# Kernel optimization log

Measured on AMD Instinct MI355X. Metric: run time of the kernel, lower is better.

Reference implementation:

```python
import jax, jax.numpy as jnp
import numpy as np

N, E, D, L = 50000, 600000, 128, 2  # nodes, edges, hidden_dim, num_gnn_layers
NEG_SLOPE = 0.2  # PyG GATv2Conv default negative_slope


def setup_inputs() -> dict:
    key = jax.random.key(0)
    ks = jax.random.split(key, 10)
    s = 1.0 / np.sqrt(D)
    return {
        "x": jax.random.normal(ks[0], (N, D), jnp.float32),
        "edge_index": jax.random.randint(ks[1], (2, E), 0, N, dtype=jnp.int32),
        # per-layer GATv2 params (stacked over L layers)
        "Wl": jax.random.normal(ks[2], (L, D, D), jnp.float32) * s,  # lin_l (source)
        "bl": jnp.zeros((L, D), jnp.float32),
        "Wr": jax.random.normal(ks[3], (L, D, D), jnp.float32) * s,  # lin_r (target)
        "br": jnp.zeros((L, D), jnp.float32),
        "att": jax.random.normal(ks[4], (L, D), jnp.float32) * s,
        "bias": jnp.zeros((L, D), jnp.float32),
        # shared residual Linear
        "W_res": jax.random.normal(ks[5], (D, D), jnp.float32) * s,
        "b_res": jnp.zeros((D,), jnp.float32),
    }


def reference(x, edge_index, Wl, bl, Wr, br, att, bias, W_res, b_res):
    n = x.shape[0]
    # add self loops (PyG GATv2Conv default add_self_loops=True)
    loops = jnp.arange(n, dtype=edge_index.dtype)
    src = jnp.concatenate([edge_index[0], loops])  # source j (messages)
    dst = jnp.concatenate([edge_index[1], loops])  # target i (aggregation)

    def conv(h, i):
        xl = h @ Wl[i] + bl[i]  # [N, D] source transform
        xr = h @ Wr[i] + br[i]  # [N, D] target transform
        m = xl[src] + xr[dst]   # [E+N, D] gathered edge messages
        e = jnp.einsum('ed,d->e', jnp.where(m > 0, m, NEG_SLOPE * m), att[i])
        # segment softmax over incoming edges of each destination node
        emax = jax.lax.stop_gradient(jax.ops.segment_max(e, dst, num_segments=n))
        ex = jnp.exp(e - emax[dst])
        denom = jax.ops.segment_sum(ex, dst, num_segments=n)
        alpha = ex / (denom[dst] + 1e-16)
        out = jax.ops.segment_sum(alpha[:, None] * xl[src], dst, num_segments=n)
        return out + bias[i]

    for i in range(Wl.shape[0]):
        x = jax.nn.relu(conv(x, i) + x @ W_res + b_res)
    return x
```

## Files before the change

kernel.cpp:

```cpp
#include <hip/hip_runtime.h>
#include <math.h>


#define DIM 128
#define NEG_SLOPE 0.2f
#define TPW 4

typedef __attribute__((ext_vector_type(8))) short short8;
typedef __attribute__((ext_vector_type(4))) float floatx4;
typedef __attribute__((ext_vector_type(2))) float f32x2;

static __device__ __forceinline__ unsigned short f2b(float f) {
    unsigned u = __float_as_uint(f);
    unsigned r = (u + 0x7FFFu + ((u >> 16) & 1u)) >> 16;
    return (unsigned short)r;
}
static __device__ __forceinline__ f32x2 cvt2(unsigned u) {
    f32x2 r;
    r.x = __uint_as_float(u << 16);
    r.y = __uint_as_float(u & 0xffff0000u);
    return r;
}
static __device__ __forceinline__ f32x2 pk_add(f32x2 a, f32x2 b) {
    f32x2 d;
    asm("v_pk_add_f32 %0, %1, %2" : "=v"(d) : "v"(a), "v"(b));
    return d;
}
static __device__ __forceinline__ f32x2 pk_mul(f32x2 a, f32x2 b) {
    f32x2 d;
    asm("v_pk_mul_f32 %0, %1, %2" : "=v"(d) : "v"(a), "v"(b));
    return d;
}
static __device__ __forceinline__ f32x2 pk_fma(f32x2 a, f32x2 b, f32x2 c) {
    f32x2 d;
    asm("v_pk_fma_f32 %0, %1, %2, %3" : "=v"(d) : "v"(a), "v"(b), "v"(c));
    return d;
}
static __device__ __forceinline__ f32x2 pk_abs2(f32x2 a) {
    f32x2 r;
    r.x = __builtin_fabsf(a.x);
    r.y = __builtin_fabsf(a.y);
    return r;
}

__global__ void k_init_counts(int* __restrict__ counts, int n) {
    int i = blockIdx.x * blockDim.x + threadIdx.x;
    if (i < n) counts[i] = 1;
}

__global__ void k_count(const int* __restrict__ dst, int E, int* __restrict__ counts) {
    int k = blockIdx.x * blockDim.x + threadIdx.x;
    if (k < E) atomicAdd(&counts[dst[k]], 1);
}

__global__ void k_scan1(const int* __restrict__ counts, int n,
                        int* __restrict__ rowptr, int* __restrict__ bsum) {
    __shared__ int s[256];
    int tid = threadIdx.x;
    int i = blockIdx.x * 256 + tid;
    int v = (i < n) ? counts[i] : 0;
    s[tid] = v;
    __syncthreads();
    for (int off = 1; off < 256; off <<= 1) {
        int t = (tid >= off) ? s[tid - off] : 0;
        __syncthreads();
        s[tid] += t;
        __syncthreads();
    }
    if (i < n) rowptr[i + 1] = s[tid];
    if (tid == 255) bsum[blockIdx.x] = s[255];
}

__global__ void k_scan2(int* __restrict__ bsum, int nb) {
    __shared__ int s[256];
    int tid = threadIdx.x;
    int v = (tid < nb) ? bsum[tid] : 0;
    s[tid] = v;
    __syncthreads();
    for (int off = 1; off < 256; off <<= 1) {
        int t = (tid >= off) ? s[tid - off] : 0;
        __syncthreads();
        s[tid] += t;
        __syncthreads();
    }
    if (tid < nb) bsum[tid] = s[tid];
}

__global__ void k_scan3(int* __restrict__ rowptr, const int* __restrict__ bsum,
                        int n, int* __restrict__ counts_to_cursors) {
    int i = blockIdx.x * 256 + threadIdx.x;
    if (i < n) {
        int add = (blockIdx.x > 0) ? bsum[blockIdx.x - 1] : 0;
        int cnt = counts_to_cursors[i];
        int v = rowptr[i + 1] + add;
        rowptr[i + 1] = v;
        counts_to_cursors[i] = v - cnt;
    }
    if (i == 0) rowptr[0] = 0;
}

__global__ void k_scatter(const int* __restrict__ src, const int* __restrict__ dst,
                          int E, int n, int* __restrict__ cur, int* __restrict__ srt) {
    int k = blockIdx.x * blockDim.x + threadIdx.x;
    int tot = E + n;
    if (k >= tot) return;
    int s, d;
    if (k < E) { s = src[k]; d = dst[k]; }
    else       { s = k - E;  d = s; }
    int p = atomicAdd(&cur[d], 1);
    srt[p] = s;
}

__global__ void k_pre(const float* __restrict__ Wl, const float* __restrict__ Wr,
                      const float* __restrict__ Wres, unsigned short* __restrict__ wfrag,
                      const float* __restrict__ h, unsigned short* __restrict__ hfrag,
                      int n, int ntiles) {
    int blk = blockIdx.x;
    if (blk < 48) {
        int idx = blk * 256 + threadIdx.x;
        int lane = idx & 63;
        int nr   = (idx >> 6) & 7;
        int ks   = (idx >> 9) & 3;
        int v    = idx >> 11;
        int sec = v % 3, l = v / 3;
        const float* W = (sec == 0) ? (Wl + l * DIM * DIM)
                       : (sec == 1) ? (Wr + l * DIM * DIM) : Wres;
        int nn = nr * 16 + (lane & 15);
        int k0 = ks * 32 + ((lane >> 4) << 3);
        ushort4 a, b;
        a.x = f2b(W[(k0 + 0) * DIM + nn]); a.y = f2b(W[(k0 + 1) * DIM + nn]);
        a.z = f2b(W[(k0 + 2) * DIM + nn]); a.w = f2b(W[(k0 + 3) * DIM + nn]);
        b.x = f2b(W[(k0 + 4) * DIM + nn]); b.y = f2b(W[(k0 + 5) * DIM + nn]);
        b.z = f2b(W[(k0 + 6) * DIM + nn]); b.w = f2b(W[(k0 + 7) * DIM + nn]);
        *(ushort4*)(wfrag + (size_t)idx * 8) = a;
        *(ushort4*)(wfrag + (size_t)idx * 8 + 4) = b;
    } else {
        int idx = (blk - 48) * 256 + threadIdx.x;
        if (idx >= ntiles * 256) return;
        int lane = idx & 63;
        int ks   = (idx >> 6) & 3;
        int tile = idx >> 8;
        int row  = tile * 16 + (lane & 15);
        int col0 = ks * 32 + ((lane >> 4) << 3);
        ushort4 a = {0, 0, 0, 0}, b = {0, 0, 0, 0};
        if (row < n) {
            float4 v0 = *(const float4*)(h + (size_t)row * DIM + col0);
            float4 v1 = *(const float4*)(h + (size_t)row * DIM + col0 + 4);
            a.x = f2b(v0.x); a.y = f2b(v0.y); a.z = f2b(v0.z); a.w = f2b(v0.w);
            b.x = f2b(v1.x); b.y = f2b(v1.y); b.z = f2b(v1.z); b.w = f2b(v1.w);
        }
        *(ushort4*)(hfrag + (size_t)idx * 8) = a;
        *(ushort4*)(hfrag + (size_t)idx * 8 + 4) = b;
    }
}

__global__ __launch_bounds__(256, 2) void k_gemm(
    const unsigned short* __restrict__ hfrag, const unsigned short* __restrict__ wfrag,
    const float* __restrict__ bl, const float* __restrict__ br, const float* __restrict__ bres,
    unsigned short* __restrict__ XLb, unsigned short* __restrict__ XRb,
    float* __restrict__ RES, int ntiles)
{
    int sec  = blockIdx.y;
    int lane = threadIdx.x & 63;
    int w    = threadIdx.x >> 6;

    const unsigned short* wbase = wfrag + (size_t)sec * (4 * 8 * 64 * 8);
    short8 bf[4][8];
#pragma unroll
    for (int ks = 0; ks < 4; ks++)
#pragma unroll
        for (int nr = 0; nr < 8; nr++)
            bf[ks][nr] = *(const short8*)(wbase + (((ks * 8 + nr) * 64 + lane) << 3));

    const float* bias = (sec == 0) ? bl : (sec == 1) ? br : bres;
    int colb = (lane >> 4) << 2;
    float4 bv[8];
#pragma unroll
    for (int nr = 0; nr < 8; nr++) bv[nr] = *(const float4*)(bias + nr * 16 + colb);

    int wid = blockIdx.x * 4 + w;
#pragma unroll
    for (int i = 0; i < TPW; i++) {
        int t = wid * TPW + i;
        if (t >= ntiles) break;
        short8 a[4];
#pragma unroll
        for (int ks = 0; ks < 4; ks++)
            a[ks] = *(const short8*)(hfrag + (((t * 4 + ks) * 64 + lane) << 3));
        floatx4 acc[8];
#pragma unroll
        for (int nr = 0; nr < 8; nr++) acc[nr] = (floatx4){0.f, 0.f, 0.f, 0.f};
#pragma unroll
        for (int ks = 0; ks < 4; ks++)
#pragma unroll
            for (int nr = 0; nr < 8; nr++)
                acc[nr] = __builtin_amdgcn_mfma_f32_16x16x32_bf16(bf[ks][nr], a[ks], acc[nr], 0, 0, 0);

        int row = t * 16 + (lane & 15);
        size_t rb = (size_t)row * DIM;
#pragma unroll
        for (int nr = 0; nr < 8; nr++) {
            float4 o;
            o.x = acc[nr][0] + bv[nr].x;
            o.y = acc[nr][1] + bv[nr].y;
            o.z = acc[nr][2] + bv[nr].z;
            o.w = acc[nr][3] + bv[nr].w;
            int col = nr * 16 + colb;
            if (sec == 2) {
                *(float4*)(RES + rb + col) = o;
            } else {
                ushort4 u;
                u.x = f2b(o.x); u.y = f2b(o.y); u.z = f2b(o.z); u.w = f2b(o.w);
                if (sec == 0) *(ushort4*)(XLb + rb + col) = u;
                else          *(ushort4*)(XRb + rb + col) = u;
            }
        }
    }
}

#define EDGE_LOGIT(K, JOFF)                                              \
    f32x2 v01_##K = cvt2(e##K.x), v23_##K = cvt2(e##K.y);                \
    f32x2 t01_##K = pk_add(v01_##K, x01);                                \
    f32x2 t23_##K = pk_add(v23_##K, x23);                                \
    f32x2 pp_##K = pk_mul(a6_01, t01_##K);                               \
    pp_##K = pk_fma(a4_01, pk_abs2(t01_##K), pp_##K);                    \
    pp_##K = pk_fma(a6_23, t23_##K, pp_##K);                             \
    pp_##K = pk_fma(a4_23, pk_abs2(t23_##K), pp_##K);                    \
    float p##K = pp_##K.x + pp_##K.y;                                    \
    p##K = (j + JOFF < se) ? p##K : -3.0e38f;

__global__ __launch_bounds__(256) void k_aggr(
    const unsigned short* __restrict__ XLb, const unsigned short* __restrict__ XRb,
    const float* __restrict__ RES, const float* __restrict__ att,
    const float* __restrict__ bias, const int* __restrict__ rowptr,
    const int* __restrict__ srt, float* __restrict__ outF,
    unsigned short* __restrict__ fragOut, int writeFrag, int n)
{
    int wave = threadIdx.x >> 6;
    int lane = threadIdx.x & 63;
    int node = blockIdx.x * 4 + wave;
    if (node >= n) return;
    int half = lane >> 5, sl = lane & 31;
    int d0 = sl << 2;

    float a0 = att[d0], a1 = att[d0 + 1], a2 = att[d0 + 2], a3 = att[d0 + 3];
    f32x2 a6_01 = {0.6f * a0, 0.6f * a1}, a6_23 = {0.6f * a2, 0.6f * a3};
    f32x2 a4_01 = {0.4f * a0, 0.4f * a1}, a4_23 = {0.4f * a2, 0.4f * a3};

    uint2 xru = *(const uint2*)(XRb + (size_t)node * DIM + d0);
    f32x2 x01 = cvt2(xru.x), x23 = cvt2(xru.y);

    int beg = rowptr[node], end = rowptr[node + 1];
    int len = end - beg;
    int hl = (len + 1) >> 1;
    int sb = beg + half * hl;
    int se = half ? end : (beg + hl);

    const uint2* R = (const uint2*)XLb;

    float m = -INFINITY, den = 0.f;
    float ax = 0.f, ay = 0.f, az = 0.f, aw = 0.f;

    for (int j = sb; j < se; j += 8) {
        int4 sA = *(const int4*)(srt + j);
        int4 sB = *(const int4*)(srt + j + 4);
        int i0 = sA.x;
        int i1 = (j + 1 < se) ? sA.y : i0;
        int i2 = (j + 2 < se) ? sA.z : i0;
        int i3 = (j + 3 < se) ? sA.w : i0;
        int i4 = (j + 4 < se) ? sB.x : i0;
        int i5 = (j + 5 < se) ? sB.y : i0;
        int i6 = (j + 6 < se) ? sB.z : i0;
        int i7 = (j + 7 < se) ? sB.w : i0;
        uint2 e0 = R[(size_t)i0 * 32 + sl];
        uint2 e1 = R[(size_t)i1 * 32 + sl];
        uint2 e2 = R[(size_t)i2 * 32 + sl];
        uint2 e3 = R[(size_t)i3 * 32 + sl];
        uint2 e4 = R[(size_t)i4 * 32 + sl];
        uint2 e5 = R[(size_t)i5 * 32 + sl];
        uint2 e6 = R[(size_t)i6 * 32 + sl];
        uint2 e7 = R[(size_t)i7 * 32 + sl];
        EDGE_LOGIT(0, 0) EDGE_LOGIT(1, 1) EDGE_LOGIT(2, 2) EDGE_LOGIT(3, 3)
        EDGE_LOGIT(4, 4) EDGE_LOGIT(5, 5) EDGE_LOGIT(6, 6) EDGE_LOGIT(7, 7)
#pragma unroll
        for (int off = 16; off >= 1; off >>= 1) {
            p0 += __shfl_xor(p0, off); p1 += __shfl_xor(p1, off);
            p2 += __shfl_xor(p2, off); p3 += __shfl_xor(p3, off);
            p4 += __shfl_xor(p4, off); p5 += __shfl_xor(p5, off);
            p6 += __shfl_xor(p6, off); p7 += __shfl_xor(p7, off);
        }
        float pm = fmaxf(fmaxf(fmaxf(p0, p1), fmaxf(p2, p3)),
                         fmaxf(fmaxf(p4, p5), fmaxf(p6, p7)));
        float mn = fmaxf(m, pm);
        float c  = __expf(m - mn);
        float w0 = __expf(p0 - mn), w1 = __expf(p1 - mn);
        float w2 = __expf(p2 - mn), w3 = __expf(p3 - mn);
        float w4 = __expf(p4 - mn), w5 = __expf(p5 - mn);
        float w6 = __expf(p6 - mn), w7 = __expf(p7 - mn);
        ax = ax * c + w0 * v01_0.x + w1 * v01_1.x + w2 * v01_2.x + w3 * v01_3.x
                    + w4 * v01_4.x + w5 * v01_5.x + w6 * v01_6.x + w7 * v01_7.x;
        ay = ay * c + w0 * v01_0.y + w1 * v01_1.y + w2 * v01_2.y + w3 * v01_3.y
                    + w4 * v01_4.y + w5 * v01_5.y + w6 * v01_6.y + w7 * v01_7.y;
        az = az * c + w0 * v23_0.x + w1 * v23_1.x + w2 * v23_2.x + w3 * v23_3.x
                    + w4 * v23_4.x + w5 * v23_5.x + w6 * v23_6.x + w7 * v23_7.x;
        aw = aw * c + w0 * v23_0.y + w1 * v23_1.y + w2 * v23_2.y + w3 * v23_3.y
                    + w4 * v23_4.y + w5 * v23_5.y + w6 * v23_6.y + w7 * v23_7.y;
        den = den * c + (((w0 + w1) + (w2 + w3)) + ((w4 + w5) + (w6 + w7)));
        m = mn;
    }

    float om   = __shfl_xor(m, 32);
    float oden = __shfl_xor(den, 32);
    float ox = __shfl_xor(ax, 32), oy = __shfl_xor(ay, 32);
    float oz = __shfl_xor(az, 32), ow = __shfl_xor(aw, 32);
    float M  = fmaxf(m, om);
    float se_ = __expf(m - M), so = __expf(om - M);
    float D  = den * se_ + oden * so + 1e-16f;
    float inv = 1.f / D;

    float4 r4 = *(const float4*)(RES + (size_t)node * DIM + d0);
    float4 b4 = *(const float4*)(bias + d0);
    float4 o;
    o.x = fmaxf((ax * se_ + ox * so) * inv + b4.x + r4.x, 0.f);
    o.y = fmaxf((ay * se_ + oy * so) * inv + b4.y + r4.y, 0.f);
    o.z = fmaxf((az * se_ + oz * so) * inv + b4.z + r4.z, 0.f);
    o.w = fmaxf((aw * se_ + ow * so) * inv + b4.w + r4.w, 0.f);

    if (half == 0) {
        if (writeFrag) {
            int tile = node >> 4;
            int ks = sl >> 3;
            int li = (node & 15) + (((sl >> 1) & 3) << 4);
            int j0 = (sl & 1) << 2;
            ushort4 u;
            u.x = f2b(o.x); u.y = f2b(o.y); u.z = f2b(o.z); u.w = f2b(o.w);
            *(ushort4*)(fragOut + ((size_t)((tile * 4 + ks) * 64 + li) << 3) + j0) = u;
        } else {
            *(float4*)(outF + (size_t)node * DIM + d0) = o;
        }
    }
}

extern "C" void kernel_launch(void* const* d_in, const int* in_sizes, int n_in,
                              void* d_out, int out_size, void* d_ws, size_t ws_size,
                              hipStream_t stream) {
    const float* x    = (const float*)d_in[0];
    const int*   ei   = (const int*)d_in[1];
    const float* Wl   = (const float*)d_in[2];
    const float* bl   = (const float*)d_in[3];
    const float* Wr   = (const float*)d_in[4];
    const float* br   = (const float*)d_in[5];
    const float* att  = (const float*)d_in[6];
    const float* bias = (const float*)d_in[7];
    const float* Wres = (const float*)d_in[8];
    const float* bres = (const float*)d_in[9];

    int n = in_sizes[0] / DIM;
    int E = in_sizes[1] / 2;
    int ntiles = (n + 15) >> 4;
    const int* srcIdx = ei;
    const int* dstIdx = ei + E;

    float* resb = (float*)d_ws;
    unsigned short* xlb   = (unsigned short*)(resb + (size_t)n * DIM);
    unsigned short* xrb   = xlb + (size_t)n * DIM;
    unsigned short* hfrag = xrb + (size_t)n * DIM;
    unsigned short* wfrag = hfrag + (size_t)ntiles * 16 * DIM;
    int* rowptr = (int*)(wfrag + 2 * 3 * DIM * DIM);
    int* tmpc   = rowptr + (n + 1);
    int* srt    = tmpc + n;
    int* bsum   = srt + (E + n + 8);

    int nb1 = (n + 255) / 256;

    k_pre<<<48 + ntiles, 256, 0, stream>>>(Wl, Wr, Wres, wfrag, x, hfrag, n, ntiles);
    k_init_counts<<<nb1, 256, 0, stream>>>(tmpc, n);
    k_count<<<(E + 255) / 256, 256, 0, stream>>>(dstIdx, E, tmpc);
    k_scan1<<<nb1, 256, 0, stream>>>(tmpc, n, rowptr, bsum);
    k_scan2<<<1, 256, 0, stream>>>(bsum, nb1);
    k_scan3<<<nb1, 256, 0, stream>>>(rowptr, bsum, n, tmpc);
    k_scatter<<<(E + n + 255) / 256, 256, 0, stream>>>(srcIdx, dstIdx, E, n, tmpc, srt);

    int gx = (ntiles + 4 * TPW - 1) / (4 * TPW);
    for (int l = 0; l < 2; l++) {
        dim3 g(gx, 3);
        k_gemm<<<g, 256, 0, stream>>>(hfrag, wfrag + (size_t)l * 3 * 4 * 8 * 64 * 8,
                                      bl + (size_t)l * DIM, br + (size_t)l * DIM, bres,
                                      xlb, xrb, resb, ntiles);
        k_aggr<<<(n + 3) / 4, 256, 0, stream>>>(xlb, xrb, resb, att + (size_t)l * DIM,
                                                bias + (size_t)l * DIM, rowptr, srt,
                                                (float*)d_out, hfrag, (l == 0) ? 1 : 0, n);
    }
}
```

Measured before the change: 242.0 us.

## Restructure edge aggregation to eight lanes per edge without online max

```diff
diff --git a/kernel.cpp b/kernel.cpp
--- a/kernel.cpp
+++ b/kernel.cpp
@@ -35,12 +35,6 @@
     f32x2 d;
     asm("v_pk_fma_f32 %0, %1, %2, %3" : "=v"(d) : "v"(a), "v"(b), "v"(c));
     return d;
-}
-static __device__ __forceinline__ f32x2 pk_abs2(f32x2 a) {
-    f32x2 r;
-    r.x = __builtin_fabsf(a.x);
-    r.y = __builtin_fabsf(a.y);
-    return r;
 }
 
 __global__ void k_init_counts(int* __restrict__ counts, int n) {
@@ -218,17 +212,6 @@
     }
 }
 
-#define EDGE_LOGIT(K, JOFF)                                              \
-    f32x2 v01_##K = cvt2(e##K.x), v23_##K = cvt2(e##K.y);                \
-    f32x2 t01_##K = pk_add(v01_##K, x01);                                \
-    f32x2 t23_##K = pk_add(v23_##K, x23);                                \
-    f32x2 pp_##K = pk_mul(a6_01, t01_##K);                               \
-    pp_##K = pk_fma(a4_01, pk_abs2(t01_##K), pp_##K);                    \
-    pp_##K = pk_fma(a6_23, t23_##K, pp_##K);                             \
-    pp_##K = pk_fma(a4_23, pk_abs2(t23_##K), pp_##K);                    \
-    float p##K = pp_##K.x + pp_##K.y;                                    \
-    p##K = (j + JOFF < se) ? p##K : -3.0e38f;
-
 __global__ __launch_bounds__(256) void k_aggr(
     const unsigned short* __restrict__ XLb, const unsigned short* __restrict__ XRb,
     const float* __restrict__ RES, const float* __restrict__ att,
@@ -240,103 +223,125 @@
     int lane = threadIdx.x & 63;
     int node = blockIdx.x * 4 + wave;
     if (node >= n) return;
-    int half = lane >> 5, sl = lane & 31;
-    int d0 = sl << 2;
-
-    float a0 = att[d0], a1 = att[d0 + 1], a2 = att[d0 + 2], a3 = att[d0 + 3];
-    f32x2 a6_01 = {0.6f * a0, 0.6f * a1}, a6_23 = {0.6f * a2, 0.6f * a3};
-    f32x2 a4_01 = {0.4f * a0, 0.4f * a1}, a4_23 = {0.4f * a2, 0.4f * a3};
-
-    uint2 xru = *(const uint2*)(XRb + (size_t)node * DIM + d0);
-    f32x2 x01 = cvt2(xru.x), x23 = cvt2(xru.y);
+    int g = lane >> 3;
+    int i = lane & 7;
+    int dbase = i << 4;
+
+    f32x2 av[8];
+    {
+        float4 t0 = *(const float4*)(att + dbase);
+        float4 t1 = *(const float4*)(att + dbase + 4);
+        float4 t2 = *(const float4*)(att + dbase + 8);
+        float4 t3 = *(const float4*)(att + dbase + 12);
+        av[0] = (f32x2){t0.x, t0.y}; av[1] = (f32x2){t0.z, t0.w};
+        av[2] = (f32x2){t1.x, t1.y}; av[3] = (f32x2){t1.z, t1.w};
+        av[4] = (f32x2){t2.x, t2.y}; av[5] = (f32x2){t2.z, t2.w};
+        av[6] = (f32x2){t3.x, t3.y}; av[7] = (f32x2){t3.z, t3.w};
+    }
+    f32x2 xv[8];
+    {
+        uint4 u0 = *(const uint4*)(XRb + (size_t)node * DIM + dbase);
+        uint4 u1 = *(const uint4*)(XRb + (size_t)node * DIM + dbase + 8);
+        xv[0] = cvt2(u0.x); xv[1] = cvt2(u0.y); xv[2] = cvt2(u0.z); xv[3] = cvt2(u0.w);
+        xv[4] = cvt2(u1.x); xv[5] = cvt2(u1.y); xv[6] = cvt2(u1.z); xv[7] = cvt2(u1.w);
+    }
+    const f32x2 c06 = {0.6f, 0.6f};
+    const f32x2 c04 = {0.4f, 0.4f};
+
+    f32x2 acc[8];
+#pragma unroll
+    for (int k = 0; k < 8; k++) acc[k] = (f32x2){0.f, 0.f};
+    float den = 0.f;
 
     int beg = rowptr[node], end = rowptr[node + 1];
-    int len = end - beg;
-    int hl = (len + 1) >> 1;
-    int sb = beg + half * hl;
-    int se = half ? end : (beg + hl);
-
-    const uint2* R = (const uint2*)XLb;
-
-    float m = -INFINITY, den = 0.f;
-    float ax = 0.f, ay = 0.f, az = 0.f, aw = 0.f;
-
-    for (int j = sb; j < se; j += 8) {
-        int4 sA = *(const int4*)(srt + j);
-        int4 sB = *(const int4*)(srt + j + 4);
-        int i0 = sA.x;
-        int i1 = (j + 1 < se) ? sA.y : i0;
-        int i2 = (j + 2 < se) ? sA.z : i0;
-        int i3 = (j + 3 < se) ? sA.w : i0;
-        int i4 = (j + 4 < se) ? sB.x : i0;
-        int i5 = (j + 5 < se) ? sB.y : i0;
-        int i6 = (j + 6 < se) ? sB.z : i0;
-        int i7 = (j + 7 < se) ? sB.w : i0;
-        uint2 e0 = R[(size_t)i0 * 32 + sl];
-        uint2 e1 = R[(size_t)i1 * 32 + sl];
-        uint2 e2 = R[(size_t)i2 * 32 + sl];
-        uint2 e3 = R[(size_t)i3 * 32 + sl];
-        uint2 e4 = R[(size_t)i4 * 32 + sl];
-        uint2 e5 = R[(size_t)i5 * 32 + sl];
-        uint2 e6 = R[(size_t)i6 * 32 + sl];
-        uint2 e7 = R[(size_t)i7 * 32 + sl];
-        EDGE_LOGIT(0, 0) EDGE_LOGIT(1, 1) EDGE_LOGIT(2, 2) EDGE_LOGIT(3, 3)
-        EDGE_LOGIT(4, 4) EDGE_LOGIT(5, 5) EDGE_LOGIT(6, 6) EDGE_LOGIT(7, 7)
-#pragma unroll
-        for (int off = 16; off >= 1; off >>= 1) {
-            p0 += __shfl_xor(p0, off); p1 += __shfl_xor(p1, off);
-            p2 += __shfl_xor(p2, off); p3 += __shfl_xor(p3, off);
-            p4 += __shfl_xor(p4, off); p5 += __shfl_xor(p5, off);
-            p6 += __shfl_xor(p6, off); p7 += __shfl_xor(p7, off);
-        }
-        float pm = fmaxf(fmaxf(fmaxf(p0, p1), fmaxf(p2, p3)),
-                         fmaxf(fmaxf(p4, p5), fmaxf(p6, p7)));
-        float mn = fmaxf(m, pm);
-        float c  = __expf(m - mn);
-        float w0 = __expf(p0 - mn), w1 = __expf(p1 - mn);
-        float w2 = __expf(p2 - mn), w3 = __expf(p3 - mn);
-        float w4 = __expf(p4 - mn), w5 = __expf(p5 - mn);
-        float w6 = __expf(p6 - mn), w7 = __expf(p7 - mn);
-        ax = ax * c + w0 * v01_0.x + w1 * v01_1.x + w2 * v01_2.x + w3 * v01_3.x
-                    + w4 * v01_4.x + w5 * v01_5.x + w6 * v01_6.x + w7 * v01_7.x;
-        ay = ay * c + w0 * v01_0.y + w1 * v01_1.y + w2 * v01_2.y + w3 * v01_3.y
-                    + w4 * v01_4.y + w5 * v01_5.y + w6 * v01_6.y + w7 * v01_7.y;
-        az = az * c + w0 * v23_0.x + w1 * v23_1.x + w2 * v23_2.x + w3 * v23_3.x
-                    + w4 * v23_4.x + w5 * v23_5.x + w6 * v23_6.x + w7 * v23_7.x;
-        aw = aw * c + w0 * v23_0.y + w1 * v23_1.y + w2 * v23_2.y + w3 * v23_3.y
-                    + w4 * v23_4.y + w5 * v23_5.y + w6 * v23_6.y + w7 * v23_7.y;
-        den = den * c + (((w0 + w1) + (w2 + w3)) + ((w4 + w5) + (w6 + w7)));
-        m = mn;
-    }
-
-    float om   = __shfl_xor(m, 32);
-    float oden = __shfl_xor(den, 32);
-    float ox = __shfl_xor(ax, 32), oy = __shfl_xor(ay, 32);
-    float oz = __shfl_xor(az, 32), ow = __shfl_xor(aw, 32);
-    float M  = fmaxf(m, om);
-    float se_ = __expf(m - M), so = __expf(om - M);
-    float D  = den * se_ + oden * so + 1e-16f;
-    float inv = 1.f / D;
-
-    float4 r4 = *(const float4*)(RES + (size_t)node * DIM + d0);
-    float4 b4 = *(const float4*)(bias + d0);
-    float4 o;
-    o.x = fmaxf((ax * se_ + ox * so) * inv + b4.x + r4.x, 0.f);
-    o.y = fmaxf((ay * se_ + oy * so) * inv + b4.y + r4.y, 0.f);
-    o.z = fmaxf((az * se_ + oz * so) * inv + b4.z + r4.z, 0.f);
-    o.w = fmaxf((aw * se_ + ow * so) * inv + b4.w + r4.w, 0.f);
-
-    if (half == 0) {
-        if (writeFrag) {
-            int tile = node >> 4;
-            int ks = sl >> 3;
-            int li = (node & 15) + (((sl >> 1) & 3) << 4);
-            int j0 = (sl & 1) << 2;
-            ushort4 u;
-            u.x = f2b(o.x); u.y = f2b(o.y); u.z = f2b(o.z); u.w = f2b(o.w);
-            *(ushort4*)(fragOut + ((size_t)((tile * 4 + ks) * 64 + li) << 3) + j0) = u;
-        } else {
-            *(float4*)(outF + (size_t)node * DIM + d0) = o;
+    for (int jb = beg; jb < end; jb += 8) {
+        int jj = jb + g;
+        int s = srt[(jj < end) ? jj : (end - 1)];
+        uint4 u0 = *(const uint4*)(XLb + (size_t)s * DIM + dbase);
+        uint4 u1 = *(const uint4*)(XLb + (size_t)s * DIM + dbase + 8);
+        f32x2 vv[8];
+        vv[0] = cvt2(u0.x); vv[1] = cvt2(u0.y); vv[2] = cvt2(u0.z); vv[3] = cvt2(u0.w);
+        vv[4] = cvt2(u1.x); vv[5] = cvt2(u1.y); vv[6] = cvt2(u1.z); vv[7] = cvt2(u1.w);
+        f32x2 pp = {0.f, 0.f};
+#pragma unroll
+        for (int k = 0; k < 8; k++) {
+            f32x2 t = pk_add(vv[k], xv[k]);
+            f32x2 ab;
+            ab.x = __builtin_fabsf(t.x);
+            ab.y = __builtin_fabsf(t.y);
+            f32x2 lk = pk_mul(c04, ab);
+            lk = pk_fma(c06, t, lk);
+            pp = pk_fma(av[k], lk, pp);
+        }
+        float p = pp.x + pp.y;
+        p += __shfl_xor(p, 1);
+        p += __shfl_xor(p, 2);
+        p += __shfl_xor(p, 4);
+        p = fminf(p, 80.f);
+        float w = __expf(p);
+        if (jj >= end) w = 0.f;
+        den += w;
+        f32x2 wp = {w, w};
+#pragma unroll
+        for (int k = 0; k < 8; k++) acc[k] = pk_fma(wp, vv[k], acc[k]);
+    }
+
+#pragma unroll
+    for (int off = 8; off <= 32; off <<= 1) {
+        den += __shfl_xor(den, off);
+#pragma unroll
+        for (int k = 0; k < 8; k++) {
+            f32x2 o;
+            o.x = __shfl_xor(acc[k].x, off);
+            o.y = __shfl_xor(acc[k].y, off);
+            acc[k] = pk_add(acc[k], o);
+        }
+    }
+
+    if (g) return;
+    float inv = 1.f / (den + 1e-16f);
+    float4 rr[4], bb[4];
+#pragma unroll
+    for (int q = 0; q < 4; q++) {
+        rr[q] = *(const float4*)(RES + (size_t)node * DIM + dbase + 4 * q);
+        bb[q] = *(const float4*)(bias + dbase + 4 * q);
+    }
+    float of[16];
+#pragma unroll
+    for (int k = 0; k < 8; k++) {
+        of[2 * k]     = acc[k].x * inv;
+        of[2 * k + 1] = acc[k].y * inv;
+    }
+#pragma unroll
+    for (int q = 0; q < 4; q++) {
+        of[4 * q + 0] = fmaxf(of[4 * q + 0] + bb[q].x + rr[q].x, 0.f);
+        of[4 * q + 1] = fmaxf(of[4 * q + 1] + bb[q].y + rr[q].y, 0.f);
+        of[4 * q + 2] = fmaxf(of[4 * q + 2] + bb[q].z + rr[q].z, 0.f);
+        of[4 * q + 3] = fmaxf(of[4 * q + 3] + bb[q].w + rr[q].w, 0.f);
+    }
+
+    if (writeFrag) {
+        int tile = node >> 4, r16 = node & 15;
+        int c0 = 2 * i, c1 = 2 * i + 1;
+        unsigned short* p0 = fragOut +
+            ((size_t)((tile * 4 + (c0 >> 2)) * 64 + r16 + ((c0 & 3) << 4)) << 3);
+        unsigned short* p1 = fragOut +
+            ((size_t)((tile * 4 + (c1 >> 2)) * 64 + r16 + ((c1 & 3) << 4)) << 3);
+        ushort4 ua, ub;
+        ua.x = f2b(of[0]);  ua.y = f2b(of[1]);  ua.z = f2b(of[2]);  ua.w = f2b(of[3]);
+        ub.x = f2b(of[4]);  ub.y = f2b(of[5]);  ub.z = f2b(of[6]);  ub.w = f2b(of[7]);
+        *(ushort4*)p0 = ua;
+        *(ushort4*)(p0 + 4) = ub;
+        ua.x = f2b(of[8]);  ua.y = f2b(of[9]);  ua.z = f2b(of[10]); ua.w = f2b(of[11]);
+        ub.x = f2b(of[12]); ub.y = f2b(of[13]); ub.z = f2b(of[14]); ub.w = f2b(of[15]);
+        *(ushort4*)p1 = ua;
+        *(ushort4*)(p1 + 4) = ub;
+    } else {
+        float* po = outF + (size_t)node * DIM + dbase;
+#pragma unroll
+        for (int q = 0; q < 4; q++) {
+            float4 o = make_float4(of[4 * q], of[4 * q + 1], of[4 * q + 2], of[4 * q + 3]);
+            *(float4*)(po + 4 * q) = o;
         }
     }
 }
```

Measured after the change: 263.9 us. +9.0%, slower.
